# Kernel optimization log

Measured on AMD Instinct MI355X. Metric: run time of the kernel, lower is better.

## Reference

```python
import jax, jax.numpy as jnp
import numpy as np

B, M, N, L = 8, 384, 1536, 20  # batch, checks (detectors), error mechanisms, BP layers
ROW_W = 8  # check-node degree of sparse parity-check matrix H


def setup_inputs() -> dict:
    key = jax.random.key(0)
    ks = jax.random.split(key, 10)
    # Sparse binary check matrix: each row has exactly ROW_W ones (LDPC-like DEM).
    rng = np.random.default_rng(0)
    H_np = np.zeros((M, N), np.float32)
    for i in range(M):
        H_np[i, rng.choice(N, ROW_W, replace=False)] = 1.0
    H = jnp.asarray(H_np)
    llrs = jax.random.uniform(ks[0], (N,), minval=0.5, maxval=2.0)
    syndromes = jax.random.randint(ks[1], (B, M, 1), 0, 2).astype(jnp.float32)
    errors = jax.random.randint(ks[2], (B, N), 0, 2).astype(jnp.float32)
    # Per-layer learned weights (damped so 20 BP iterations stay numerically stable).
    weights_de = jax.random.uniform(ks[3], (L, M, N), minval=0.1, maxval=0.25)
    weights_llr = jax.random.uniform(ks[4], (L, N), minval=0.5, maxval=1.0)
    marg_weights_de = jax.random.uniform(ks[5], (M, N), minval=0.5, maxval=1.0)
    marg_weights_llr = jax.random.uniform(ks[6], (N,), minval=0.5, maxval=1.0)
    residual_weights = jax.random.uniform(ks[7], (L,), minval=0.0, maxval=0.1)
    rhos = jnp.ones((L,), jnp.float32) / L  # init: ones normalized by layers
    return dict(syndromes=syndromes, errors=errors, H=H, llrs=llrs,
                weights_de=weights_de, weights_llr=weights_llr,
                marg_weights_de=marg_weights_de, marg_weights_llr=marg_weights_llr,
                residual_weights=residual_weights, rhos=rhos)


def reference(syndromes, errors, H, llrs, weights_de, weights_llr,
              marg_weights_de, marg_weights_llr, residual_weights, rhos):
    sign = (1.0 - 2.0 * syndromes) * H          # (B,M,N): (-1)^syndrome masked by H
    one_minus_e = 1.0 - errors                  # (B,N)

    def step(msg_dn, per_layer):
        w_de, w_llr, res_w, rho = per_layer
        # --- error (variable) node update ---
        base = H * (llrs * w_llr)                                     # (M,N)
        msg_en = (base + jnp.sum(msg_dn * w_de, axis=1, keepdims=True)) * H - msg_dn
        # --- detector (check) node update: tanh-product with self-exclusion by division ---
        d = jnp.tanh(msg_en * 0.5)
        d = jnp.where(d == 0.0, 1.0, d)
        p = jnp.prod(d, axis=2, keepdims=True)                        # (B,M,1)
        msg_dn_new = 2.0 * jnp.arctanh(p / d) * sign + res_w * msg_dn
        # --- marginals (beliefs) + per-layer loss ---
        beliefs = jnp.sum(msg_dn_new * marg_weights_de, axis=1) + llrs * marg_weights_llr  # (B,N)
        loss_b = jnp.sum(jax.nn.softplus(beliefs) - one_minus_e * beliefs, axis=1) * rho   # (B,)
        return msg_dn_new, loss_b

    msg0 = jnp.zeros((syndromes.shape[0], H.shape[0], H.shape[1]), jnp.float32)
    _, losses = jax.lax.scan(step, msg0, (weights_de, weights_llr, residual_weights, rhos))
    return jnp.sum(losses) / syndromes.shape[0]  # scalar mean-over-batch loss
```

## Files before the change

kernel.cpp:

```cpp
#include <hip/hip_runtime.h>
#include <math.h>

#define MB 8
#define MM 384
#define NN 1536
#define LL 20
#define RW 8
#define HE 4
#define NE (MM*RW)
#define NT 768
#define VP 12
#define VG 3

#define LOG2E 1.44269504f
#define LN2   0.69314718f

#define SOFT_BAR() asm volatile("s_waitcnt lgkmcnt(0)\n\ts_barrier" ::: "memory")

static __device__ __forceinline__ float dpp_xor1(float x) {
    return __int_as_float(
        __builtin_amdgcn_mov_dpp(__float_as_int(x), 0xB1, 0xF, 0xF, true));
}

__global__ __launch_bounds__(256) void setup_kernel(
    const float* __restrict__ H,
    const float* __restrict__ llrs,
    const float* __restrict__ w_llr,
    const float* __restrict__ w_de,
    const float* __restrict__ marg_de,
    int*   __restrict__ col_pack,
    float* __restrict__ base_e,
    float* __restrict__ wde_vT,
    float* __restrict__ marg_vT,
    int*   __restrict__ gcnt,
    float* __restrict__ out) {
    const int m = blockIdx.x;
    const int t = threadIdx.x;
    const int w = t >> 6, lane = t & 63;
    __shared__ int s_qcol[4][RW];
    __shared__ int s_qcnt[4];
    __shared__ int s_col[RW];
    __shared__ int s_pos[RW];

    const float* row = H + (size_t)m * NN;
    int count = 0;
    for (int c0 = w * 384; c0 < (w + 1) * 384; c0 += 64) {
        float v = row[c0 + lane];
        unsigned long long mask = __ballot(v != 0.0f);
        if (v != 0.0f) {
            int pos = count + (int)__popcll(mask & ((1ull << lane) - 1ull));
            if (pos < RW) s_qcol[w][pos] = c0 + lane;
        }
        count += (int)__popcll(mask);
    }
    if (lane == 0) s_qcnt[w] = (count < RW) ? count : RW;
    __syncthreads();
    if (t == 0) {
        int off = 0;
        for (int q = 0; q < 4; ++q)
            for (int i = 0; i < s_qcnt[q]; ++i) {
                if (off < RW) s_col[off] = s_qcol[q][i];
                ++off;
            }
    }
    __syncthreads();

    if (t < RW) {
        int c = s_col[t];
        int pos = atomicAdd(&gcnt[c], 1);
        if (pos >= VP) pos = VP - 1;
        s_pos[t] = pos;
        col_pack[m * RW + t] = c | (pos << 16);
        marg_vT[((pos >> 2) * NN + c) * 4 + (pos & 3)] = marg_de[m * NN + c] * LN2;
    }
    if (m == 0 && t == 0) out[0] = 0.0f;
    __syncthreads();

    for (int idx = t; idx < LL * RW; idx += 256) {
        int l = idx >> 3;
        int k = idx & 7;
        int c = s_col[k];
        int pos = s_pos[k];
        wde_vT[((l * VG + (pos >> 2)) * NN + c) * 4 + (pos & 3)] =
            w_de[(size_t)l * MM * NN + (size_t)m * NN + c];
        base_e[l * NE + m * RW + k] = llrs[c] * w_llr[l * NN + c] * LOG2E;
    }
}

#define LAYER_BODY(lv, WC0, WC1, BC, WN0, WN1, BN)                            \
{                                                                             \
    float bel0 = bias[0], bel1 = bias[1];                                     \
    {             \
        float S0, S1;                                                         \
        {          \
            float4 a = ((const float4*)s_cN)[t];                              \
            S0    = a.x*WC0[0] + a.y*WC0[1] + a.z*WC0[2] + a.w*WC0[3];        \
            bel0 += a.x*mg0[0] + a.y*mg0[1] + a.z*mg0[2] + a.w*mg0[3];        \
            float4 c4 = ((const float4*)s_cN)[t + NT];                        \
            S1    = c4.x*WC1[0] + c4.y*WC1[1] + c4.z*WC1[2] + c4.w*WC1[3];    \
            bel1 += c4.x*mg1[0] + c4.y*mg1[1] + c4.z*mg1[2] + c4.w*mg1[3];    \
        }                                                                     \
        if (deg0 > 4) {                                                       \
            float4 a = ((const float4*)s_cN)[NN + t];                         \
            S0   += a.x*WC0[4] + a.y*WC0[5] + a.z*WC0[6] + a.w*WC0[7];        \
            bel0 += a.x*mg0[4] + a.y*mg0[5] + a.z*mg0[6] + a.w*mg0[7];        \
        }                                                                     \
        if (deg1 > 4) {                                                       \
            float4 c4 = ((const float4*)s_cN)[NN + t + NT];                   \
            S1   += c4.x*WC1[4] + c4.y*WC1[5] + c4.z*WC1[6] + c4.w*WC1[7];    \
            bel1 += c4.x*mg1[4] + c4.y*mg1[5] + c4.z*mg1[6] + c4.w*mg1[7];    \
        }                                                                     \
        if (deg0 > 8) {                                                       \
            float4 a = ((const float4*)s_cN)[2 * NN + t];                     \
            S0   += a.x*WC0[8] + a.y*WC0[9] + a.z*WC0[10] + a.w*WC0[11];      \
            bel0 += a.x*mg0[8] + a.y*mg0[9] + a.z*mg0[10] + a.w*mg0[11];      \
        }                                                                     \
        if (deg1 > 8) {                                                       \
            float4 c4 = ((const float4*)s_cN)[2 * NN + t + NT];               \
            S1   += c4.x*WC1[8] + c4.y*WC1[9] + c4.z*WC1[10] + c4.w*WC1[11];  \
            bel1 += c4.x*mg1[8] + c4.y*mg1[9] + c4.z*mg1[10] + c4.w*mg1[11];  \
        }                                                                     \
        s_S[t]      = S0;                                                     \
        s_S[t + NT] = S1;                                                     \
    }                                                                         \
    SOFT_BAR();                \
    {                                                                         \
                                     \
        float ss[HE];                                                         \
        _Pragma("unroll")                                                     \
        for (int k = 0; k < HE; ++k) ss[k] = s_S[col[k]];                     \
                        \
        if ((lv) > 0) {                                                       \
            const float rr = rhos[(lv) - 1];                                  \
            float sp0 = fmaxf(bel0, 0.0f) + __logf(1.0f + __expf(-fabsf(bel0))); \
            float sp1 = fmaxf(bel1, 0.0f) + __logf(1.0f + __expf(-fabsf(bel1))); \
            loss += rr * ((sp0 - omeg[0] * bel0) + (sp1 - omeg[1] * bel1));   \
        }                                                                     \
               \
        {                                                                     \
            int lb = ((lv) + 1 < LL) ? ((lv) + 1) : (LL - 1);                 \
            _Pragma("unroll")                                                 \
            for (int jg = 0; jg < VG; ++jg) {                                 \
                float4 a = ((const float4*)wde_vT)[(lb * VG + jg) * NN + t];  \
                WN0[jg*4+0]=a.x; WN0[jg*4+1]=a.y; WN0[jg*4+2]=a.z; WN0[jg*4+3]=a.w; \
                float4 c4 = ((const float4*)wde_vT)[(lb * VG + jg) * NN + t + NT]; \
                WN1[jg*4+0]=c4.x; WN1[jg*4+1]=c4.y; WN1[jg*4+2]=c4.z; WN1[jg*4+3]=c4.w; \
            }                                                                 \
            const float4 bp4 = ((const float4*)(base_e_g + lb * NE))[t];      \
            BN[0]=bp4.x; BN[1]=bp4.y; BN[2]=bp4.z; BN[3]=bp4.w;               \
        }                                                                     \
        const float rw_ = res_w[(lv)];                                        \
        float d[HE];                                                          \
        _Pragma("unroll")                                                     \
        for (int k = 0; k < HE; ++k) {                                        \
            float te = BC[k] + ss[k] - msg[k];               \
            float e  = __builtin_amdgcn_exp2f(te);                            \
            float dd = 1.0f - 2.0f * __builtin_amdgcn_rcpf(e + 1.0f);         \
            dd = fminf(fmaxf(dd, -1.0f), 1.0f);                               \
            if (dd == 0.0f) dd = 1.0f;                                        \
            d[k] = dd;                                                        \
        }                                                                     \
        float pre2 = d[0] * d[1];                                             \
        float suf1 = d[2] * d[3];                                             \
        float p4   = pre2 * suf1;                                             \
        float pot  = dpp_xor1(p4);                                            \
        float ex[HE];                                                         \
        ex[0] = d[1] * suf1;                                                  \
        ex[1] = d[0] * suf1;                                                  \
        ex[2] = pre2 * d[3];                                                  \
        ex[3] = pre2 * d[2];                                                  \
        _Pragma("unroll")                                                     \
        for (int k = 0; k < HE; ++k) {                                        \
            float x  = ex[k] * pot;                                           \
            float la = __builtin_amdgcn_logf(1.0f + x);                       \
            float lb2 = __builtin_amdgcn_logf(1.0f - x);                      \
            float nm = sgn * (la - lb2) + rw_ * msg[k];      \
            msg[k] = nm;                                                      \
            s_cN[esl[k]] = nm;                                                \
        }                                                                     \
    }                                                                         \
    SOFT_BAR();                  \
}

__global__ __launch_bounds__(NT) void bp_kernel(
    const float* __restrict__ synd,
    const float* __restrict__ errors,
    const float* __restrict__ llrs,
    const float* __restrict__ marg_llr,
    const float* __restrict__ res_w,
    const float* __restrict__ rhos,
    const int*   __restrict__ col_pack,
    const float* __restrict__ base_e_g,
    const float* __restrict__ wde_vT,
    const float* __restrict__ marg_vT,
    const int*   __restrict__ gdeg,
    float* __restrict__ out) {

    __shared__ float s_cN[NN * VP];
    __shared__ float s_S[NN];
    __shared__ float s_red[12];

    const int b = blockIdx.x;
    const int t = threadIdx.x;
    const int m = t >> 1;

    int col[HE], esl[HE];
    {
        const int4 cp = ((const int4*)col_pack)[t];
        int v[HE] = {cp.x, cp.y, cp.z, cp.w};
        #pragma unroll
        for (int k = 0; k < HE; ++k) {
            int c = v[k] & 0xFFFF, pos = v[k] >> 16;
            col[k] = c;
            esl[k] = ((pos >> 2) * NN + c) * 4 + (pos & 3);
        }
    }
    float msg[HE] = {0.0f, 0.0f, 0.0f, 0.0f};
    const float sgn = 1.0f - 2.0f * synd[b * MM + m];

    const int deg0 = gdeg[t];
    const int deg1 = gdeg[t + NT];
    float bias[2], omeg[2];
    #pragma unroll
    for (int i = 0; i < 2; ++i) {
        int n = t + i * NT;
        bias[i] = llrs[n] * marg_llr[n];
        omeg[i] = 1.0f - errors[b * NN + n];
    }

    float mg0[VP], mg1[VP];
    #pragma unroll
    for (int jg = 0; jg < VG; ++jg) {
        float4 a = ((const float4*)marg_vT)[jg * NN + t];
        mg0[jg*4+0] = a.x; mg0[jg*4+1] = a.y; mg0[jg*4+2] = a.z; mg0[jg*4+3] = a.w;
        float4 c4 = ((const float4*)marg_vT)[jg * NN + t + NT];
        mg1[jg*4+0] = c4.x; mg1[jg*4+1] = c4.y; mg1[jg*4+2] = c4.z; mg1[jg*4+3] = c4.w;
    }
    float wcA0[VP], wcA1[VP], wcB0[VP], wcB1[VP];
    #pragma unroll
    for (int jg = 0; jg < VG; ++jg) {
        float4 a = ((const float4*)wde_vT)[jg * NN + t];
        wcA0[jg*4+0] = a.x; wcA0[jg*4+1] = a.y; wcA0[jg*4+2] = a.z; wcA0[jg*4+3] = a.w;
        float4 c4 = ((const float4*)wde_vT)[jg * NN + t + NT];
        wcA1[jg*4+0] = c4.x; wcA1[jg*4+1] = c4.y; wcA1[jg*4+2] = c4.z; wcA1[jg*4+3] = c4.w;
    }
    float bcA[HE], bcB[HE];
    {
        const float4 bp4 = ((const float4*)base_e_g)[t];
        bcA[0] = bp4.x; bcA[1] = bp4.y; bcA[2] = bp4.z; bcA[3] = bp4.w;
    }

    #pragma unroll
    for (int j = 0; j < 6; ++j)
        ((float4*)s_cN)[j * NT + t] = make_float4(0.f, 0.f, 0.f, 0.f);

    float loss = 0.0f;
    __syncthreads();

    for (int l = 0; l < LL; l += 2) {
        LAYER_BODY(l,     wcA0, wcA1, bcA, wcB0, wcB1, bcB);
        LAYER_BODY(l + 1, wcB0, wcB1, bcB, wcA0, wcA1, bcA);
    }

    {
        const float rr = rhos[LL - 1];
        float bel0 = bias[0], bel1 = bias[1];
        {
            float4 a = ((const float4*)s_cN)[t];
            bel0 += a.x*mg0[0] + a.y*mg0[1] + a.z*mg0[2] + a.w*mg0[3];
            float4 c4 = ((const float4*)s_cN)[t + NT];
            bel1 += c4.x*mg1[0] + c4.y*mg1[1] + c4.z*mg1[2] + c4.w*mg1[3];
        }
        if (deg0 > 4) {
            float4 a = ((const float4*)s_cN)[NN + t];
            bel0 += a.x*mg0[4] + a.y*mg0[5] + a.z*mg0[6] + a.w*mg0[7];
        }
        if (deg1 > 4) {
            float4 c4 = ((const float4*)s_cN)[NN + t + NT];
            bel1 += c4.x*mg1[4] + c4.y*mg1[5] + c4.z*mg1[6] + c4.w*mg1[7];
        }
        if (deg0 > 8) {
            float4 a = ((const float4*)s_cN)[2 * NN + t];
            bel0 += a.x*mg0[8] + a.y*mg0[9] + a.z*mg0[10] + a.w*mg0[11];
        }
        if (deg1 > 8) {
            float4 c4 = ((const float4*)s_cN)[2 * NN + t + NT];
            bel1 += c4.x*mg1[8] + c4.y*mg1[9] + c4.z*mg1[10] + c4.w*mg1[11];
        }
        float sp0 = fmaxf(bel0, 0.0f) + __logf(1.0f + __expf(-fabsf(bel0)));
        float sp1 = fmaxf(bel1, 0.0f) + __logf(1.0f + __expf(-fabsf(bel1)));
        loss += rr * ((sp0 - omeg[0] * bel0) + (sp1 - omeg[1] * bel1));
    }

    #pragma unroll
    for (int off = 32; off > 0; off >>= 1)
        loss += __shfl_down(loss, off, 64);
    int wave = t >> 6, lane = t & 63;
    if (lane == 0) s_red[wave] = loss;
    __syncthreads();
    if (t == 0) {
        float tot = 0.0f;
        #pragma unroll
        for (int w = 0; w < 12; ++w) tot += s_red[w];
        atomicAdd(out, tot * (1.0f / (float)MB));
    }
}

extern "C" void kernel_launch(void* const* d_in, const int* in_sizes, int n_in,
                              void* d_out, int out_size, void* d_ws, size_t ws_size,
                              hipStream_t stream) {
    const float* synd     = (const float*)d_in[0];
    const float* errors   = (const float*)d_in[1];
    const float* H        = (const float*)d_in[2];
    const float* llrs     = (const float*)d_in[3];
    const float* w_de     = (const float*)d_in[4];
    const float* w_llr    = (const float*)d_in[5];
    const float* marg_de  = (const float*)d_in[6];
    const float* marg_llr = (const float*)d_in[7];
    const float* res_w    = (const float*)d_in[8];
    const float* rhos     = (const float*)d_in[9];
    float* out = (float*)d_out;

    float* wde_vT  = (float*)d_ws;
    float* marg_vT = wde_vT + (size_t)LL * VG * NN * 4;
    int*   gcnt    = (int*)(marg_vT + VG * NN * 4);
    float* base_e  = (float*)(gcnt + NN);
    int*   col_pack= (int*)(base_e + (size_t)LL * NE);

    hipMemsetAsync(gcnt, 0, NN * sizeof(int), stream);
    setup_kernel<<<MM, 256, 0, stream>>>(H, llrs, w_llr, w_de, marg_de,
                                         col_pack, base_e, wde_vT, marg_vT,
                                         gcnt, out);
    bp_kernel<<<MB, NT, 0, stream>>>(synd, errors, llrs, marg_llr, res_w, rhos,
                                     col_pack, base_e, wde_vT, marg_vT, gcnt, out);
}
```

Baseline: 141.2 us.

## Swizzle variable-slot layout, hoist next-layer weight prefetch, defer belief accumulation

XORs the low two bits of each edge's slot index with column bits, so the shared-memory message slots and the transposed weight/marginal layouts are permuted to spread LDS bank accesses. Moves the global prefetch of next-layer weights and base terms to the top of each layer, before the first barrier, so it has longer to overlap. Defers the first belief partial sum until after the barrier and precomputes base-minus-message in registers at the end of the previous layer. These changes add register pressure from keeping g0a/g0b and tm live across the barrier.

```diff
diff --git a/kernel.cpp b/kernel.cpp
--- a/kernel.cpp
+++ b/kernel.cpp
@@ -69,9 +69,10 @@
         int c = s_col[t];
         int pos = atomicAdd(&gcnt[c], 1);
         if (pos >= VP) pos = VP - 1;
-        s_pos[t] = pos;
-        col_pack[m * RW + t] = c | (pos << 16);
-        marg_vT[((pos >> 2) * NN + c) * 4 + (pos & 3)] = marg_de[m * NN + c] * LN2;
+        int ps = (pos & ~3) | ((pos & 3) ^ ((c >> 3) & 3));
+        s_pos[t] = ps;
+        col_pack[m * RW + t] = c | (ps << 16);
+        marg_vT[((ps >> 2) * NN + c) * 4 + (ps & 3)] = marg_de[m * NN + c] * LN2;
     }
     if (m == 0 && t == 0) out[0] = 0.0f;
     __syncthreads();
@@ -80,80 +81,80 @@
         int l = idx >> 3;
         int k = idx & 7;
         int c = s_col[k];
-        int pos = s_pos[k];
-        wde_vT[((l * VG + (pos >> 2)) * NN + c) * 4 + (pos & 3)] =
+        int ps = s_pos[k];
+        wde_vT[((l * VG + (ps >> 2)) * NN + c) * 4 + (ps & 3)] =
             w_de[(size_t)l * MM * NN + (size_t)m * NN + c];
         base_e[l * NE + m * RW + k] = llrs[c] * w_llr[l * NN + c] * LOG2E;
     }
 }
 
-#define LAYER_BODY(lv, WC0, WC1, BC, WN0, WN1, BN)                            \
+#define LAYER_BODY(lv, WC0, WC1, WN0, WN1, BN)                                \
 {                                                                             \
-    float bel0 = bias[0], bel1 = bias[1];                                     \
-    {             \
-        float S0, S1;                                                         \
-        {          \
-            float4 a = ((const float4*)s_cN)[t];                              \
-            S0    = a.x*WC0[0] + a.y*WC0[1] + a.z*WC0[2] + a.w*WC0[3];        \
-            bel0 += a.x*mg0[0] + a.y*mg0[1] + a.z*mg0[2] + a.w*mg0[3];        \
-            float4 c4 = ((const float4*)s_cN)[t + NT];                        \
-            S1    = c4.x*WC1[0] + c4.y*WC1[1] + c4.z*WC1[2] + c4.w*WC1[3];    \
-            bel1 += c4.x*mg1[0] + c4.y*mg1[1] + c4.z*mg1[2] + c4.w*mg1[3];    \
-        }                                                                     \
+      \
+    {                                                                         \
+        int lb = ((lv) + 1 < LL) ? ((lv) + 1) : (LL - 1);                     \
+        _Pragma("unroll")                                                     \
+        for (int jg = 0; jg < VG; ++jg) {                                     \
+            float4 a = ((const float4*)wde_vT)[(lb * VG + jg) * NN + t];      \
+            WN0[jg*4+0]=a.x; WN0[jg*4+1]=a.y; WN0[jg*4+2]=a.z; WN0[jg*4+3]=a.w; \
+            float4 c4 = ((const float4*)wde_vT)[(lb * VG + jg) * NN + t + NT];\
+            WN1[jg*4+0]=c4.x; WN1[jg*4+1]=c4.y; WN1[jg*4+2]=c4.z; WN1[jg*4+3]=c4.w; \
+        }                                                                     \
+        const float4 bp4 = ((const float4*)(base_e_g + lb * NE))[t];          \
+        BN[0]=bp4.x; BN[1]=bp4.y; BN[2]=bp4.z; BN[3]=bp4.w;                   \
+    }                                                                         \
+                 \
+    float4 g0a = ((const float4*)s_cN)[t];                                    \
+    float4 g0b = ((const float4*)s_cN)[t + NT];                               \
+    float belx0 = bias[0], belx1 = bias[1];                                   \
+    {                                                                         \
+        float S0 = g0a.x*WC0[0] + g0a.y*WC0[1] + g0a.z*WC0[2] + g0a.w*WC0[3]; \
+        float S1 = g0b.x*WC1[0] + g0b.y*WC1[1] + g0b.z*WC1[2] + g0b.w*WC1[3]; \
         if (deg0 > 4) {                                                       \
             float4 a = ((const float4*)s_cN)[NN + t];                         \
-            S0   += a.x*WC0[4] + a.y*WC0[5] + a.z*WC0[6] + a.w*WC0[7];        \
-            bel0 += a.x*mg0[4] + a.y*mg0[5] + a.z*mg0[6] + a.w*mg0[7];        \
+            S0    += a.x*WC0[4] + a.y*WC0[5] + a.z*WC0[6] + a.w*WC0[7];       \
+            belx0 += a.x*mg0[4] + a.y*mg0[5] + a.z*mg0[6] + a.w*mg0[7];       \
         }                                                                     \
         if (deg1 > 4) {                                                       \
             float4 c4 = ((const float4*)s_cN)[NN + t + NT];                   \
-            S1   += c4.x*WC1[4] + c4.y*WC1[5] + c4.z*WC1[6] + c4.w*WC1[7];    \
-            bel1 += c4.x*mg1[4] + c4.y*mg1[5] + c4.z*mg1[6] + c4.w*mg1[7];    \
+            S1    += c4.x*WC1[4] + c4.y*WC1[5] + c4.z*WC1[6] + c4.w*WC1[7];   \
+            belx1 += c4.x*mg1[4] + c4.y*mg1[5] + c4.z*mg1[6] + c4.w*mg1[7];   \
         }                                                                     \
         if (deg0 > 8) {                                                       \
             float4 a = ((const float4*)s_cN)[2 * NN + t];                     \
-            S0   += a.x*WC0[8] + a.y*WC0[9] + a.z*WC0[10] + a.w*WC0[11];      \
-            bel0 += a.x*mg0[8] + a.y*mg0[9] + a.z*mg0[10] + a.w*mg0[11];      \
+            S0    += a.x*WC0[8] + a.y*WC0[9] + a.z*WC0[10] + a.w*WC0[11];     \
+            belx0 += a.x*mg0[8] + a.y*mg0[9] + a.z*mg0[10] + a.w*mg0[11];     \
         }                                                                     \
         if (deg1 > 8) {                                                       \
             float4 c4 = ((const float4*)s_cN)[2 * NN + t + NT];               \
-            S1   += c4.x*WC1[8] + c4.y*WC1[9] + c4.z*WC1[10] + c4.w*WC1[11];  \
-            bel1 += c4.x*mg1[8] + c4.y*mg1[9] + c4.z*mg1[10] + c4.w*mg1[11];  \
+            S1    += c4.x*WC1[8] + c4.y*WC1[9] + c4.z*WC1[10] + c4.w*WC1[11]; \
+            belx1 += c4.x*mg1[8] + c4.y*mg1[9] + c4.z*mg1[10] + c4.w*mg1[11]; \
         }                                                                     \
         s_S[t]      = S0;                                                     \
         s_S[t + NT] = S1;                                                     \
     }                                                                         \
-    SOFT_BAR();                \
+    SOFT_BAR();      \
     {                                                                         \
                                      \
         float ss[HE];                                                         \
         _Pragma("unroll")                                                     \
         for (int k = 0; k < HE; ++k) ss[k] = s_S[col[k]];                     \
-                        \
+                            \
         if ((lv) > 0) {                                                       \
             const float rr = rhos[(lv) - 1];                                  \
+            float bel0 = belx0 + g0a.x*mg0[0] + g0a.y*mg0[1]                  \
+                               + g0a.z*mg0[2] + g0a.w*mg0[3];                 \
+            float bel1 = belx1 + g0b.x*mg1[0] + g0b.y*mg1[1]                  \
+                               + g0b.z*mg1[2] + g0b.w*mg1[3];                 \
             float sp0 = fmaxf(bel0, 0.0f) + __logf(1.0f + __expf(-fabsf(bel0))); \
             float sp1 = fmaxf(bel1, 0.0f) + __logf(1.0f + __expf(-fabsf(bel1))); \
             loss += rr * ((sp0 - omeg[0] * bel0) + (sp1 - omeg[1] * bel1));   \
         }                                                                     \
-               \
-        {                                                                     \
-            int lb = ((lv) + 1 < LL) ? ((lv) + 1) : (LL - 1);                 \
-            _Pragma("unroll")                                                 \
-            for (int jg = 0; jg < VG; ++jg) {                                 \
-                float4 a = ((const float4*)wde_vT)[(lb * VG + jg) * NN + t];  \
-                WN0[jg*4+0]=a.x; WN0[jg*4+1]=a.y; WN0[jg*4+2]=a.z; WN0[jg*4+3]=a.w; \
-                float4 c4 = ((const float4*)wde_vT)[(lb * VG + jg) * NN + t + NT]; \
-                WN1[jg*4+0]=c4.x; WN1[jg*4+1]=c4.y; WN1[jg*4+2]=c4.z; WN1[jg*4+3]=c4.w; \
-            }                                                                 \
-            const float4 bp4 = ((const float4*)(base_e_g + lb * NE))[t];      \
-            BN[0]=bp4.x; BN[1]=bp4.y; BN[2]=bp4.z; BN[3]=bp4.w;               \
-        }                                                                     \
         const float rw_ = res_w[(lv)];                                        \
         float d[HE];                                                          \
         _Pragma("unroll")                                                     \
         for (int k = 0; k < HE; ++k) {                                        \
-            float te = BC[k] + ss[k] - msg[k];               \
+            float te = tm[k] + ss[k];                        \
             float e  = __builtin_amdgcn_exp2f(te);                            \
             float dd = 1.0f - 2.0f * __builtin_amdgcn_rcpf(e + 1.0f);         \
             dd = fminf(fmaxf(dd, -1.0f), 1.0f);                               \
@@ -178,6 +179,9 @@
             msg[k] = nm;                                                      \
             s_cN[esl[k]] = nm;                                                \
         }                                                                     \
+                        \
+        _Pragma("unroll")                                                     \
+        for (int k = 0; k < HE; ++k) tm[k] = BN[k] - msg[k];                  \
     }                                                                         \
     SOFT_BAR();                  \
 }
@@ -245,9 +249,12 @@
         wcA1[jg*4+0] = c4.x; wcA1[jg*4+1] = c4.y; wcA1[jg*4+2] = c4.z; wcA1[jg*4+3] = c4.w;
     }
     float bcA[HE], bcB[HE];
+    float tm[HE];
     {
         const float4 bp4 = ((const float4*)base_e_g)[t];
         bcA[0] = bp4.x; bcA[1] = bp4.y; bcA[2] = bp4.z; bcA[3] = bp4.w;
+        #pragma unroll
+        for (int k = 0; k < HE; ++k) tm[k] = bcA[k];
     }
 
     #pragma unroll
@@ -258,8 +265,8 @@
     __syncthreads();
 
     for (int l = 0; l < LL; l += 2) {
-        LAYER_BODY(l,     wcA0, wcA1, bcA, wcB0, wcB1, bcB);
-        LAYER_BODY(l + 1, wcB0, wcB1, bcB, wcA0, wcA1, bcA);
+        LAYER_BODY(l,     wcA0, wcA1, wcB0, wcB1, bcB);
+        LAYER_BODY(l + 1, wcB0, wcB1, wcA0, wcA1, bcA);
     }
 
     {
```

New measurement: 142.2 us. No clear change (+0.7%).
